# Optimization experiments

Hardware: AMD Instinct MI355X
Metric: run time of the kernel (lower is better)

Reference implementation:

```python
import jax, jax.numpy as jnp
import numpy as np

N, E, D, R = 50000, 625000, 128, 200
BN_EPS = 1e-5


def setup_inputs() -> dict:
    key = jax.random.key(0)
    ks = jax.random.split(key, 16)
    x = jax.random.normal(ks[0], (N, D), dtype=jnp.float32)
    r_feats = jax.random.normal(ks[1], (R, D), dtype=jnp.float32)
    src = jax.random.randint(ks[2], (E,), 0, N, dtype=jnp.int32)
    dst = jax.random.randint(ks[3], (E,), 0, N, dtype=jnp.int32)
    etype = jax.random.randint(ks[4], (E,), 0, R, dtype=jnp.int32)
    norm = jax.random.uniform(ks[5], (E, 1), dtype=jnp.float32)
    out_edges_mask = jax.random.randint(ks[6], (E,), 0, 2) == 1
    in_edges_mask = jnp.logical_not(out_edges_mask)  # masks partition edges
    s = 1.0 / np.sqrt(D)
    def lin(k):
        kw, kb = jax.random.split(k)
        return (jax.random.uniform(kw, (D, D), jnp.float32, -s, s),
                jax.random.uniform(kb, (D,), jnp.float32, -s, s))
    W_O_w, W_O_b = lin(ks[7])
    W_I_w, W_I_b = lin(ks[8])
    W_S_w, W_S_b = lin(ks[9])
    W_R_w, W_R_b = lin(ks[10])
    loop_rel = jax.random.normal(ks[11], (1, D), dtype=jnp.float32) * s  # xavier-ish
    bn_gamma = jnp.ones((D,), jnp.float32)
    bn_beta = jnp.zeros((D,), jnp.float32)
    return {"x": x, "r_feats": r_feats, "src": src, "dst": dst, "etype": etype,
            "norm": norm, "in_edges_mask": in_edges_mask, "out_edges_mask": out_edges_mask,
            "W_O_w": W_O_w, "W_O_b": W_O_b, "W_I_w": W_I_w, "W_I_b": W_I_b,
            "W_S_w": W_S_w, "W_S_b": W_S_b, "W_R_w": W_R_w, "W_R_b": W_R_b,
            "loop_rel": loop_rel, "bn_gamma": bn_gamma, "bn_beta": bn_beta}


def reference(x, r_feats, src, dst, etype, norm, in_edges_mask, out_edges_mask,
              W_O_w, W_O_b, W_I_w, W_I_b, W_S_w, W_S_b, W_R_w, W_R_b,
              loop_rel, bn_gamma, bn_beta):
    # r_feats with self-loop relation appended: [R+1, D]
    r_ext = jnp.concatenate([r_feats, loop_rel], axis=0)
    # per-edge relation feature scaled by norm: [E, D]
    e_h = r_ext[etype] * norm
    # compose (sub): u_sub_e -> src feature minus edge feature
    comp_h = x[src] - e_h
    # per-direction linear projections, selected by the edge partition masks
    h_O = comp_h @ W_O_w.T + W_O_b
    h_I = comp_h @ W_I_w.T + W_I_b
    new_comp_h = jnp.where(out_edges_mask[:, None], h_O, h_I)
    # scatter-sum messages to destination nodes: [N, D]
    agg = jax.ops.segment_sum(new_comp_h, dst, num_segments=x.shape[0])
    # self-loop branch (sub with loop relation)
    comp_h_s = x - r_ext[-1]
    n_out = (comp_h_s @ W_S_w.T + W_S_b + agg) * (1.0 / 3.0)  # dropout in eval mode
    # BatchNorm1d (training-mode batch stats, biased variance)
    mean = jnp.mean(n_out, axis=0)
    var = jnp.mean((n_out - mean) ** 2, axis=0)
    n_out = (n_out - mean) * jax.lax.rsqrt(var + BN_EPS) * bn_gamma + bn_beta
    n_out = jnp.tanh(n_out)
    r_out = r_ext @ W_R_w.T + W_R_b
    return n_out, r_out[:-1]
```

## Files before the change

kernel.cpp:

```cpp
#include <hip/hip_runtime.h>
#include <cstddef>

#define N_NODES 50000
#define N_EDGES 625000
#define DIM     128
#define R_REL   200
#define BN_EPS  1e-5f
#define SLOTS   64

typedef __bf16 bf16x8 __attribute__((ext_vector_type(8)));
typedef float  f32x4  __attribute__((ext_vector_type(4)));

__device__ __forceinline__ float bfu2f(unsigned int hi16) {
    return __uint_as_float(hi16);
}
__device__ __forceinline__ unsigned int f2bfr(float f) {
    unsigned int u = __float_as_uint(f);
    return (u + 0x7fffu + ((u >> 16) & 1u)) >> 16;
}

__global__ void detect_mask_kernel(const unsigned char* __restrict__ in_m,
                                   const unsigned char* __restrict__ out_m,
                                   int* __restrict__ flag) {
    int ok = 1;
    for (int e = 0; e < 256; ++e) ok &= (((int)in_m[e] + (int)out_m[e]) == 1);
    *flag = ok;
}

__global__ __launch_bounds__(256) void tobf16_kernel(const float* __restrict__ in,
                                                     ushort* __restrict__ out, int n4) {
    int i = blockIdx.x * 256 + threadIdx.x;
    if (i < n4) {
        float4 v = ((const float4*)in)[i];
        ushort4 o;
        o.x = (ushort)f2bfr(v.x);
        o.y = (ushort)f2bfr(v.y);
        o.z = (ushort)f2bfr(v.z);
        o.w = (ushort)f2bfr(v.w);
        ((ushort4*)out)[i] = o;
    }
}

__global__ __launch_bounds__(384) void prep_weights_kernel(
    const float* __restrict__ WO, const float* __restrict__ WI,
    const float* __restrict__ WS, ushort* __restrict__ Wb) {
    int f = blockIdx.x;
    int k = threadIdx.x;
    const float third = 1.0f / 3.0f;
    float w;
    if (k < 128)      w = WS[f * DIM + k];
    else if (k < 256) w = WO[f * DIM + (k - 128)];
    else              w = WI[f * DIM + (k - 256)];
    Wb[f * 384 + k] = (ushort)f2bfr(w * third);
}

__global__ void prep_bias_kernel(const float* __restrict__ WS, const float* __restrict__ bS,
                                 const float* __restrict__ bO, const float* __restrict__ bI,
                                 const float* __restrict__ loop,
                                 float* __restrict__ bias0, float* __restrict__ bO3,
                                 float* __restrict__ bI3) {
    int f = threadIdx.x;
    float acc = 0.f;
    for (int k = 0; k < DIM; ++k) acc += loop[k] * WS[f * DIM + k];
    const float third = 1.0f / 3.0f;
    bias0[f] = (bS[f] - acc) * third;
    bO3[f]   = bO[f] * third;
    bI3[f]   = bI[f] * third;
}

__global__ __launch_bounds__(128) void rout_kernel(const float* __restrict__ rf,
                                                   const float* __restrict__ WR,
                                                   const float* __restrict__ bR,
                                                   float* __restrict__ out) {
    int r = blockIdx.x;
    int f = threadIdx.x;
    __shared__ float row[DIM];
    row[f] = rf[r * DIM + f];
    __syncthreads();
    float acc = bR[f];
    for (int k = 0; k < DIM; ++k) acc += row[k] * WR[f * DIM + k];
    out[r * DIM + f] = acc;
}

__global__ __launch_bounds__(256) void slot_fill_kernel(
    const int* __restrict__ dst, const int* __restrict__ src,
    const int* __restrict__ et, const float* __restrict__ norm,
    const void* __restrict__ omask, const int* __restrict__ flag,
    int* __restrict__ cnt, uint2* __restrict__ erec) {
    int e = blockIdx.x * 256 + threadIdx.x;
    if (e >= N_EDGES) return;
    int fl = *flag;
    bool m = fl ? (((const unsigned char*)omask)[e] != 0)
                : (((const int*)omask)[e] != 0);
    int d = dst[e];
    int k = atomicAdd(&cnt[d], 1);
    if (k < SLOTS) {
        unsigned w0 = (unsigned)src[e] | ((unsigned)et[e] << 16) | (m ? 0x80000000u : 0u);
        erec[(size_t)d * SLOTS + k] = make_uint2(w0, (unsigned)__float_as_int(norm[e]));
    }
}

#define AGG_CALC(EX, EY, XW, RW)                                   \
    {                                                              \
        float nm = __uint_as_float(EY);                            \
        float fm = (float)((EX) >> 31);                            \
        float x0 = bfu2f((XW) << 16), x1 = bfu2f((XW) & 0xffff0000u); \
        float r0 = bfu2f((RW) << 16), r1 = bfu2f((RW) & 0xffff0000u); \
        float v0 = __builtin_fmaf(-nm, r0, x0);                    \
        float v1 = __builtin_fmaf(-nm, r1, x1);                    \
        aT0 += v0; aT1 += v1;                                      \
        aO0 = __builtin_fmaf(fm, v0, aO0);                         \
        aO1 = __builtin_fmaf(fm, v1, aO1);                         \
        cOf += fm;                                                 \
    }

__global__ __launch_bounds__(256, 8) void aggregate_kernel(
    const unsigned int* __restrict__ xb,
    const unsigned int* __restrict__ rb,
    const uint2* __restrict__ erec,
    const int* __restrict__ cnt,
    unsigned int* __restrict__ S_Ob, unsigned int* __restrict__ S_Ib,
    float* __restrict__ cntO, float* __restrict__ cntI) {
    int wv = threadIdx.x >> 6;
    unsigned lane = threadIdx.x & 63;
    int n = blockIdx.x * 4 + wv;
    if (n >= N_NODES) return;
    int deg = cnt[n];
    deg = deg < SLOTS ? deg : SLOTS;
    int beg = n * SLOTS, end = beg + deg;

    float aT0 = 0.f, aT1 = 0.f, aO0 = 0.f, aO1 = 0.f, cOf = 0.f;

    int j = beg;
    for (; j + 3 < end; j += 4) {
        uint2 e0 = erec[j], e1 = erec[j + 1], e2 = erec[j + 2], e3 = erec[j + 3];
        unsigned xw0 = xb[((e0.x & 0xffffu) << 6) + lane];
        unsigned rw0 = rb[(((e0.x >> 16) & 0x7fffu) << 6) + lane];
        unsigned xw1 = xb[((e1.x & 0xffffu) << 6) + lane];
        unsigned rw1 = rb[(((e1.x >> 16) & 0x7fffu) << 6) + lane];
        unsigned xw2 = xb[((e2.x & 0xffffu) << 6) + lane];
        unsigned rw2 = rb[(((e2.x >> 16) & 0x7fffu) << 6) + lane];
        unsigned xw3 = xb[((e3.x & 0xffffu) << 6) + lane];
        unsigned rw3 = rb[(((e3.x >> 16) & 0x7fffu) << 6) + lane];
        AGG_CALC(e0.x, e0.y, xw0, rw0)
        AGG_CALC(e1.x, e1.y, xw1, rw1)
        AGG_CALC(e2.x, e2.y, xw2, rw2)
        AGG_CALC(e3.x, e3.y, xw3, rw3)
    }
    for (; j < end; ++j) {
        uint2 e0 = erec[j];
        unsigned xw0 = xb[((e0.x & 0xffffu) << 6) + lane];
        unsigned rw0 = rb[(((e0.x >> 16) & 0x7fffu) << 6) + lane];
        AGG_CALC(e0.x, e0.y, xw0, rw0)
    }

    float aI0 = aT0 - aO0, aI1 = aT1 - aO1;
    S_Ob[((unsigned)n << 6) + lane] = f2bfr(aO0) | (f2bfr(aO1) << 16);
    S_Ib[((unsigned)n << 6) + lane] = f2bfr(aI0) | (f2bfr(aI1) << 16);
    if (lane == 0) { cntO[n] = cOf; cntI[n] = (float)deg - cOf; }
}

__global__ __launch_bounds__(256, 4) void gemm_kernel(
    const ushort* __restrict__ xb, const ushort* __restrict__ S_Ob,
    const ushort* __restrict__ S_Ib, const ushort* __restrict__ Wb,
    const float* __restrict__ bias0, const float* __restrict__ bO3,
    const float* __restrict__ bI3, const float* __restrict__ cntO,
    const float* __restrict__ cntI, float* __restrict__ y,
    float* __restrict__ colsum, float* __restrict__ colsq) {
    __shared__ ushort Bs[128][136];
    __shared__ float redS[4][128];
    __shared__ float redQ[4][128];

    int tid = threadIdx.x;
    int wv = tid >> 6, lane = tid & 63;
    int cl = lane & 15, kg = lane >> 4;
    int wrow0 = blockIdx.x * 64 + wv * 16;

    f32x4 acc[8];
#pragma unroll
    for (int cf = 0; cf < 8; ++cf) acc[cf] = (f32x4){0.f, 0.f, 0.f, 0.f};

    int rowA = wrow0 + cl;
    int rowc = rowA < N_NODES ? rowA : N_NODES - 1;
    const ushort* Abase[3] = {xb, S_Ob, S_Ib};

    for (int kq = 0; kq < 3; ++kq) {
        __syncthreads();
#pragma unroll
        for (int j = 0; j < 8; ++j) {
            int i = tid + j * 256;
            int col = i >> 4, k8 = (i & 15) << 3;
            uint4 w = *(const uint4*)(Wb + (size_t)col * 384 + kq * 128 + k8);
            *(uint4*)&Bs[col][k8] = w;
        }
        const ushort* Ap0 = Abase[kq] + (size_t)rowc * 128 + kg * 8;
        uint4 a4[4];
#pragma unroll
        for (int ks = 0; ks < 4; ++ks) a4[ks] = *(const uint4*)(Ap0 + ks * 32);
        __syncthreads();
#pragma unroll
        for (int ks = 0; ks < 4; ++ks) {
            bf16x8 af = __builtin_bit_cast(bf16x8, a4[ks]);
#pragma unroll
            for (int cf = 0; cf < 8; ++cf) {
                bf16x8 bv = __builtin_bit_cast(bf16x8,
                    *(const uint4*)&Bs[cf * 16 + cl][ks * 32 + kg * 8]);
                acc[cf] = __builtin_amdgcn_mfma_f32_16x16x32_bf16(af, bv, acc[cf], 0, 0, 0);
            }
        }
    }

    float b0a[8], boa[8], bia[8];
#pragma unroll
    for (int cf = 0; cf < 8; ++cf) {
        int col = cf * 16 + cl;
        b0a[cf] = bias0[col]; boa[cf] = bO3[col]; bia[cf] = bI3[col];
    }
    float cOv[4], cIv[4]; int rows[4]; bool rv[4];
#pragma unroll
    for (int r = 0; r < 4; ++r) {
        int row = wrow0 + kg * 4 + r;
        rows[r] = row; rv[r] = row < N_NODES;
        cOv[r] = rv[r] ? cntO[row] : 0.f;
        cIv[r] = rv[r] ? cntI[row] : 0.f;
    }
    float ps[8], pq[8];
#pragma unroll
    for (int cf = 0; cf < 8; ++cf) {
        float s = 0.f, q = 0.f;
        int col = cf * 16 + cl;
#pragma unroll
        for (int r = 0; r < 4; ++r) {
            if (rv[r]) {
                float v = acc[cf][r] + b0a[cf] + cOv[r] * boa[cf] + cIv[r] * bia[cf];
                y[(size_t)rows[r] * DIM + col] = v;
                s += v; q += v * v;
            }
        }
        s += __shfl_xor(s, 16);
        s += __shfl_xor(s, 32);
        q += __shfl_xor(q, 16);
        q += __shfl_xor(q, 32);
        ps[cf] = s; pq[cf] = q;
    }
    if (kg == 0) {
#pragma unroll
        for (int cf = 0; cf < 8; ++cf) {
            redS[wv][cf * 16 + cl] = ps[cf];
            redQ[wv][cf * 16 + cl] = pq[cf];
        }
    }
    __syncthreads();
    if (tid < 128) {
        float s = redS[0][tid] + redS[1][tid] + redS[2][tid] + redS[3][tid];
        float q = redQ[0][tid] + redQ[1][tid] + redQ[2][tid] + redQ[3][tid];
        atomicAdd(colsum + tid, s);
        atomicAdd(colsq + tid, q);
    }
}

__global__ __launch_bounds__(256) void bn_apply_kernel(
    float* __restrict__ y, const float* __restrict__ colsum, const float* __restrict__ colsq,
    const float* __restrict__ gamma, const float* __restrict__ beta) {
    __shared__ __align__(16) float sc[DIM];
    __shared__ __align__(16) float sh[DIM];
    int tid = threadIdx.x;
    if (tid < DIM) {
        float mean = colsum[tid] * (1.0f / N_NODES);
        float var  = colsq[tid] * (1.0f / N_NODES) - mean * mean;
        float s = rsqrtf(var + BN_EPS) * gamma[tid];
        sc[tid] = s;
        sh[tid] = beta[tid] - mean * s;
    }
    __syncthreads();
    const int total4 = N_NODES * 32;
    for (int i = blockIdx.x * 256 + tid; i < total4; i += gridDim.x * 256) {
        float4 s4 = ((const float4*)sc)[i & 31];
        float4 h4 = ((const float4*)sh)[i & 31];
        float4 v = ((float4*)y)[i];
        v.x = tanhf(v.x * s4.x + h4.x);
        v.y = tanhf(v.y * s4.y + h4.y);
        v.z = tanhf(v.z * s4.z + h4.z);
        v.w = tanhf(v.w * s4.w + h4.w);
        ((float4*)y)[i] = v;
    }
}

extern "C" void kernel_launch(void* const* d_in, const int* in_sizes, int n_in,
                              void* d_out, int out_size, void* d_ws, size_t ws_size,
                              hipStream_t stream) {
    const float* x        = (const float*)d_in[0];
    const float* r_feats  = (const float*)d_in[1];
    const int*   src      = (const int*)d_in[2];
    const int*   dst      = (const int*)d_in[3];
    const int*   etype    = (const int*)d_in[4];
    const float* norm     = (const float*)d_in[5];
    const void*  in_mask  = d_in[6];
    const void*  out_mask = d_in[7];
    const float* W_O_w    = (const float*)d_in[8];
    const float* W_O_b    = (const float*)d_in[9];
    const float* W_I_w    = (const float*)d_in[10];
    const float* W_I_b    = (const float*)d_in[11];
    const float* W_S_w    = (const float*)d_in[12];
    const float* W_S_b    = (const float*)d_in[13];
    const float* W_R_w    = (const float*)d_in[14];
    const float* W_R_b    = (const float*)d_in[15];
    const float* loop_rel = (const float*)d_in[16];
    const float* bn_gamma = (const float*)d_in[17];
    const float* bn_beta  = (const float*)d_in[18];

    const size_t ND = (size_t)N_NODES * DIM;
    char* p = (char*)d_ws;
    auto alloc = [&](size_t bytes) { void* r = (void*)p; p += (bytes + 255) & ~(size_t)255; return r; };

    ushort* S_Ob = (ushort*)alloc(ND * 2);
    ushort* S_Ib = (ushort*)alloc(ND * 2);
    ushort* xb   = (ushort*)alloc(ND * 2);
    ushort* rb   = (ushort*)alloc((size_t)R_REL * DIM * 2);
    uint2* erec  = (uint2*)alloc((size_t)N_NODES * SLOTS * 8);
    ushort* Wb   = (ushort*)alloc((size_t)DIM * 384 * 2);
    float* bias0 = (float*)alloc(DIM * 4);
    float* bO3   = (float*)alloc(DIM * 4);
    float* bI3   = (float*)alloc(DIM * 4);
    float* colsum= (float*)alloc(DIM * 4);
    float* colsq = (float*)alloc(DIM * 4);
    float* cntO  = (float*)alloc(N_NODES * 4);
    float* cntI  = (float*)alloc(N_NODES * 4);
    int*   cnt   = (int*)alloc(N_NODES * 4);
    int*   flag  = (int*)alloc(4);

    float* y    = (float*)d_out;
    float* rout = (float*)d_out + ND;

    hipMemsetAsync(cnt, 0, N_NODES * sizeof(int), stream);
    hipMemsetAsync(colsum, 0, DIM * sizeof(float), stream);
    hipMemsetAsync(colsq, 0, DIM * sizeof(float), stream);

    detect_mask_kernel<<<1, 1, 0, stream>>>((const unsigned char*)in_mask,
                                            (const unsigned char*)out_mask, flag);
    tobf16_kernel<<<(int)((ND / 4 + 255) / 256), 256, 0, stream>>>(x, xb, (int)(ND / 4));
    tobf16_kernel<<<(R_REL * DIM / 4 + 255) / 256, 256, 0, stream>>>(r_feats, rb, R_REL * DIM / 4);
    prep_weights_kernel<<<128, 384, 0, stream>>>(W_O_w, W_I_w, W_S_w, Wb);
    prep_bias_kernel<<<1, 128, 0, stream>>>(W_S_w, W_S_b, W_O_b, W_I_b, loop_rel,
                                            bias0, bO3, bI3);
    rout_kernel<<<R_REL, 128, 0, stream>>>(r_feats, W_R_w, W_R_b, rout);

    slot_fill_kernel<<<(N_EDGES + 255) / 256, 256, 0, stream>>>(
        dst, src, etype, norm, out_mask, flag, cnt, erec);

    aggregate_kernel<<<(N_NODES + 3) / 4, 256, 0, stream>>>(
        (const unsigned int*)xb, (const unsigned int*)rb, erec, cnt,
        (unsigned int*)S_Ob, (unsigned int*)S_Ib, cntO, cntI);

    gemm_kernel<<<(N_NODES + 63) / 64, 256, 0, stream>>>(
        xb, S_Ob, S_Ib, Wb, bias0, bO3, bI3, cntO, cntI, y, colsum, colsq);

    bn_apply_kernel<<<2048, 256, 0, stream>>>(y, colsum, colsq, bn_gamma, bn_beta);
}
```

Measured before the change: 155.2 us.

## Fuse setup kernels and memsets; process two nodes per wavefront in aggregation

Replaces three memsets, the mask-detect kernel and two bf16 conversion kernels with one init kernel, and folds the bias prep into the weight-prep kernel with a shared-memory reduction. This cuts the number of launches and serial single-thread work. The aggregation kernel now handles two nodes per 64-lane wavefront, each half-wave loading 8-byte uint2 chunks, so gathers are wider and the wavefront count is halved. The cost is divergence when the two nodes in a wavefront have different degrees.

New measurement: 147.6 us. -4.9%, faster.

```diff
diff --git a/kernel.cpp b/kernel.cpp
--- a/kernel.cpp
+++ b/kernel.cpp
@@ -7,6 +7,8 @@
 #define R_REL   200
 #define BN_EPS  1e-5f
 #define SLOTS   64
+#define ND4     ((N_NODES * DIM) / 4)
+#define R4      ((R_REL * DIM) / 4)
 
 typedef __bf16 bf16x8 __attribute__((ext_vector_type(8)));
 typedef float  f32x4  __attribute__((ext_vector_type(4)));
@@ -19,31 +21,46 @@
     return (u + 0x7fffu + ((u >> 16) & 1u)) >> 16;
 }
 
-__global__ void detect_mask_kernel(const unsigned char* __restrict__ in_m,
-                                   const unsigned char* __restrict__ out_m,
-                                   int* __restrict__ flag) {
-    int ok = 1;
-    for (int e = 0; e < 256; ++e) ok &= (((int)in_m[e] + (int)out_m[e]) == 1);
-    *flag = ok;
-}
-
-__global__ __launch_bounds__(256) void tobf16_kernel(const float* __restrict__ in,
-                                                     ushort* __restrict__ out, int n4) {
-    int i = blockIdx.x * 256 + threadIdx.x;
-    if (i < n4) {
-        float4 v = ((const float4*)in)[i];
+__global__ __launch_bounds__(256) void init_kernel(
+    const float* __restrict__ x, ushort* __restrict__ xb,
+    const float* __restrict__ rf, ushort* __restrict__ rb,
+    int* __restrict__ cnt, float* __restrict__ colsum, float* __restrict__ colsq,
+    const unsigned char* __restrict__ in_m, const unsigned char* __restrict__ out_m,
+    int* __restrict__ flag) {
+    int gid = blockIdx.x * 256 + threadIdx.x;
+    int total = gridDim.x * 256;
+    for (int i = gid; i < ND4; i += total) {
+        float4 v = ((const float4*)x)[i];
         ushort4 o;
-        o.x = (ushort)f2bfr(v.x);
-        o.y = (ushort)f2bfr(v.y);
-        o.z = (ushort)f2bfr(v.z);
-        o.w = (ushort)f2bfr(v.w);
-        ((ushort4*)out)[i] = o;
+        o.x = (ushort)f2bfr(v.x); o.y = (ushort)f2bfr(v.y);
+        o.z = (ushort)f2bfr(v.z); o.w = (ushort)f2bfr(v.w);
+        ((ushort4*)xb)[i] = o;
+    }
+    if (gid < R4) {
+        float4 v = ((const float4*)rf)[gid];
+        ushort4 o;
+        o.x = (ushort)f2bfr(v.x); o.y = (ushort)f2bfr(v.y);
+        o.z = (ushort)f2bfr(v.z); o.w = (ushort)f2bfr(v.w);
+        ((ushort4*)rb)[gid] = o;
+    }
+    for (int i = gid; i < N_NODES; i += total) cnt[i] = 0;
+    if (gid < DIM) { colsum[gid] = 0.f; colsq[gid] = 0.f; }
+    if (blockIdx.x == 0) {
+        int ok = (((int)in_m[threadIdx.x] + (int)out_m[threadIdx.x]) == 1) ? 1 : 0;
+        __shared__ int sred[4];
+        unsigned long long b = __ballot(ok);
+        if ((threadIdx.x & 63) == 0) sred[threadIdx.x >> 6] = (b == ~0ULL) ? 1 : 0;
+        __syncthreads();
+        if (threadIdx.x == 0) *flag = sred[0] & sred[1] & sred[2] & sred[3];
     }
 }
 
 __global__ __launch_bounds__(384) void prep_weights_kernel(
     const float* __restrict__ WO, const float* __restrict__ WI,
-    const float* __restrict__ WS, ushort* __restrict__ Wb) {
+    const float* __restrict__ WS, const float* __restrict__ loop,
+    const float* __restrict__ bS, const float* __restrict__ bO,
+    const float* __restrict__ bI, ushort* __restrict__ Wb,
+    float* __restrict__ bias0, float* __restrict__ bO3, float* __restrict__ bI3) {
     int f = blockIdx.x;
     int k = threadIdx.x;
     const float third = 1.0f / 3.0f;
@@ -52,20 +69,16 @@
     else if (k < 256) w = WO[f * DIM + (k - 128)];
     else              w = WI[f * DIM + (k - 256)];
     Wb[f * 384 + k] = (ushort)f2bfr(w * third);
-}
-
-__global__ void prep_bias_kernel(const float* __restrict__ WS, const float* __restrict__ bS,
-                                 const float* __restrict__ bO, const float* __restrict__ bI,
-                                 const float* __restrict__ loop,
-                                 float* __restrict__ bias0, float* __restrict__ bO3,
-                                 float* __restrict__ bI3) {
-    int f = threadIdx.x;
-    float acc = 0.f;
-    for (int k = 0; k < DIM; ++k) acc += loop[k] * WS[f * DIM + k];
-    const float third = 1.0f / 3.0f;
-    bias0[f] = (bS[f] - acc) * third;
-    bO3[f]   = bO[f] * third;
-    bI3[f]   = bI[f] * third;
+    __shared__ float red[128];
+    if (k < 128) red[k] = loop[k] * WS[f * DIM + k];
+    __syncthreads();
+    for (int off = 64; off; off >>= 1) {
+        if (k < off) red[k] += red[k + off];
+        __syncthreads();
+    }
+    if (k == 0)   bias0[f] = (bS[f] - red[0]) * third;
+    if (k == 64)  bO3[f] = bO[f] * third;
+    if (k == 128) bI3[f] = bI[f] * third;
 }
 
 __global__ __launch_bounds__(128) void rout_kernel(const float* __restrict__ rf,
@@ -100,64 +113,83 @@
     }
 }
 
-#define AGG_CALC(EX, EY, XW, RW)                                   \
-    {                                                              \
-        float nm = __uint_as_float(EY);                            \
-        float fm = (float)((EX) >> 31);                            \
-        float x0 = bfu2f((XW) << 16), x1 = bfu2f((XW) & 0xffff0000u); \
-        float r0 = bfu2f((RW) << 16), r1 = bfu2f((RW) & 0xffff0000u); \
-        float v0 = __builtin_fmaf(-nm, r0, x0);                    \
-        float v1 = __builtin_fmaf(-nm, r1, x1);                    \
-        aT0 += v0; aT1 += v1;                                      \
-        aO0 = __builtin_fmaf(fm, v0, aO0);                         \
-        aO1 = __builtin_fmaf(fm, v1, aO1);                         \
-        cOf += fm;                                                 \
+#define AGG4(E, XW, RW)                                              \
+    {                                                                \
+        float nm = __uint_as_float((E).y);                           \
+        float fm = (float)((E).x >> 31);                             \
+        float x0 = bfu2f((XW).x << 16), x1 = bfu2f((XW).x & 0xffff0000u); \
+        float x2 = bfu2f((XW).y << 16), x3 = bfu2f((XW).y & 0xffff0000u); \
+        float r0 = bfu2f((RW).x << 16), r1 = bfu2f((RW).x & 0xffff0000u); \
+        float r2 = bfu2f((RW).y << 16), r3 = bfu2f((RW).y & 0xffff0000u); \
+        float v0 = __builtin_fmaf(-nm, r0, x0);                      \
+        float v1 = __builtin_fmaf(-nm, r1, x1);                      \
+        float v2 = __builtin_fmaf(-nm, r2, x2);                      \
+        float v3 = __builtin_fmaf(-nm, r3, x3);                      \
+        aT0 += v0; aT1 += v1; aT2 += v2; aT3 += v3;                  \
+        aO0 = __builtin_fmaf(fm, v0, aO0);                           \
+        aO1 = __builtin_fmaf(fm, v1, aO1);                           \
+        aO2 = __builtin_fmaf(fm, v2, aO2);                           \
+        aO3 = __builtin_fmaf(fm, v3, aO3);                           \
+        cOf += fm;                                                   \
     }
 
 __global__ __launch_bounds__(256, 8) void aggregate_kernel(
-    const unsigned int* __restrict__ xb,
-    const unsigned int* __restrict__ rb,
+    const uint2* __restrict__ xb2,
+    const uint2* __restrict__ rb2,
     const uint2* __restrict__ erec,
     const int* __restrict__ cnt,
-    unsigned int* __restrict__ S_Ob, unsigned int* __restrict__ S_Ib,
+    uint2* __restrict__ S_Ob, uint2* __restrict__ S_Ib,
     float* __restrict__ cntO, float* __restrict__ cntI) {
     int wv = threadIdx.x >> 6;
-    unsigned lane = threadIdx.x & 63;
-    int n = blockIdx.x * 4 + wv;
-    if (n >= N_NODES) return;
-    int deg = cnt[n];
-    deg = deg < SLOTS ? deg : SLOTS;
-    int beg = n * SLOTS, end = beg + deg;
-
-    float aT0 = 0.f, aT1 = 0.f, aO0 = 0.f, aO1 = 0.f, cOf = 0.f;
-
-    int j = beg;
-    for (; j + 3 < end; j += 4) {
-        uint2 e0 = erec[j], e1 = erec[j + 1], e2 = erec[j + 2], e3 = erec[j + 3];
-        unsigned xw0 = xb[((e0.x & 0xffffu) << 6) + lane];
-        unsigned rw0 = rb[(((e0.x >> 16) & 0x7fffu) << 6) + lane];
-        unsigned xw1 = xb[((e1.x & 0xffffu) << 6) + lane];
-        unsigned rw1 = rb[(((e1.x >> 16) & 0x7fffu) << 6) + lane];
-        unsigned xw2 = xb[((e2.x & 0xffffu) << 6) + lane];
-        unsigned rw2 = rb[(((e2.x >> 16) & 0x7fffu) << 6) + lane];
-        unsigned xw3 = xb[((e3.x & 0xffffu) << 6) + lane];
-        unsigned rw3 = rb[(((e3.x >> 16) & 0x7fffu) << 6) + lane];
-        AGG_CALC(e0.x, e0.y, xw0, rw0)
-        AGG_CALC(e1.x, e1.y, xw1, rw1)
-        AGG_CALC(e2.x, e2.y, xw2, rw2)
-        AGG_CALC(e3.x, e3.y, xw3, rw3)
-    }
-    for (; j < end; ++j) {
-        uint2 e0 = erec[j];
-        unsigned xw0 = xb[((e0.x & 0xffffu) << 6) + lane];
-        unsigned rw0 = rb[(((e0.x >> 16) & 0x7fffu) << 6) + lane];
-        AGG_CALC(e0.x, e0.y, xw0, rw0)
-    }
-
-    float aI0 = aT0 - aO0, aI1 = aT1 - aO1;
-    S_Ob[((unsigned)n << 6) + lane] = f2bfr(aO0) | (f2bfr(aO1) << 16);
-    S_Ib[((unsigned)n << 6) + lane] = f2bfr(aI0) | (f2bfr(aI1) << 16);
-    if (lane == 0) { cntO[n] = cOf; cntI[n] = (float)deg - cOf; }
+    int lane = threadIdx.x & 63;
+    unsigned l5 = lane & 31;
+    int half = lane >> 5;
+    int n = (blockIdx.x * 4 + wv) * 2 + half;
+    bool valid = n < N_NODES;
+    int deg = 0;
+    if (valid) { deg = cnt[n]; deg = deg < SLOTS ? deg : SLOTS; }
+    int other = __shfl_xor(deg, 32);
+    int mdeg = deg > other ? deg : other;
+    unsigned base = (unsigned)n * SLOTS;
+
+    float aT0 = 0.f, aT1 = 0.f, aT2 = 0.f, aT3 = 0.f;
+    float aO0 = 0.f, aO1 = 0.f, aO2 = 0.f, aO3 = 0.f, cOf = 0.f;
+
+    int j = 0;
+    for (; j + 1 < mdeg; j += 2) {
+        bool a0 = j < deg, a1 = j + 1 < deg;
+        uint2 e0, e1, xw0, rw0, xw1, rw1;
+        if (a0) e0 = erec[base + j];
+        if (a1) e1 = erec[base + j + 1];
+        if (a0) {
+            xw0 = xb2[((e0.x & 0xffffu) << 5) + l5];
+            rw0 = rb2[(((e0.x >> 16) & 0x7fffu) << 5) + l5];
+        }
+        if (a1) {
+            xw1 = xb2[((e1.x & 0xffffu) << 5) + l5];
+            rw1 = rb2[(((e1.x >> 16) & 0x7fffu) << 5) + l5];
+        }
+        if (a0) AGG4(e0, xw0, rw0)
+        if (a1) AGG4(e1, xw1, rw1)
+    }
+    if (j < deg) {
+        uint2 e0 = erec[base + j];
+        uint2 xw0 = xb2[((e0.x & 0xffffu) << 5) + l5];
+        uint2 rw0 = rb2[(((e0.x >> 16) & 0x7fffu) << 5) + l5];
+        AGG4(e0, xw0, rw0)
+    }
+
+    if (valid) {
+        float aI0 = aT0 - aO0, aI1 = aT1 - aO1, aI2 = aT2 - aO2, aI3 = aT3 - aO3;
+        uint2 so, si;
+        so.x = f2bfr(aO0) | (f2bfr(aO1) << 16);
+        so.y = f2bfr(aO2) | (f2bfr(aO3) << 16);
+        si.x = f2bfr(aI0) | (f2bfr(aI1) << 16);
+        si.y = f2bfr(aI2) | (f2bfr(aI3) << 16);
+        S_Ob[((unsigned)n << 5) + l5] = so;
+        S_Ib[((unsigned)n << 5) + l5] = si;
+        if (l5 == 0) { cntO[n] = cOf; cntI[n] = (float)deg - cOf; }
+    }
 }
 
 __global__ __launch_bounds__(256, 4) void gemm_kernel(
@@ -332,25 +364,22 @@
     float* y    = (float*)d_out;
     float* rout = (float*)d_out + ND;
 
-    hipMemsetAsync(cnt, 0, N_NODES * sizeof(int), stream);
-    hipMemsetAsync(colsum, 0, DIM * sizeof(float), stream);
-    hipMemsetAsync(colsq, 0, DIM * sizeof(float), stream);
-
-    detect_mask_kernel<<<1, 1, 0, stream>>>((const unsigned char*)in_mask,
-                                            (const unsigned char*)out_mask, flag);
-    tobf16_kernel<<<(int)((ND / 4 + 255) / 256), 256, 0, stream>>>(x, xb, (int)(ND / 4));
-    tobf16_kernel<<<(R_REL * DIM / 4 + 255) / 256, 256, 0, stream>>>(r_feats, rb, R_REL * DIM / 4);
-    prep_weights_kernel<<<128, 384, 0, stream>>>(W_O_w, W_I_w, W_S_w, Wb);
-    prep_bias_kernel<<<1, 128, 0, stream>>>(W_S_w, W_S_b, W_O_b, W_I_b, loop_rel,
-                                            bias0, bO3, bI3);
+    init_kernel<<<6250, 256, 0, stream>>>(
+        x, xb, r_feats, rb, cnt, colsum, colsq,
+        (const unsigned char*)in_mask, (const unsigned char*)out_mask, flag);
+
+    prep_weights_kernel<<<128, 384, 0, stream>>>(
+        W_O_w, W_I_w, W_S_w, loop_rel, W_S_b, W_O_b, W_I_b,
+        Wb, bias0, bO3, bI3);
+
     rout_kernel<<<R_REL, 128, 0, stream>>>(r_feats, W_R_w, W_R_b, rout);
 
     slot_fill_kernel<<<(N_EDGES + 255) / 256, 256, 0, stream>>>(
         dst, src, etype, norm, out_mask, flag, cnt, erec);
 
-    aggregate_kernel<<<(N_NODES + 3) / 4, 256, 0, stream>>>(
-        (const unsigned int*)xb, (const unsigned int*)rb, erec, cnt,
-        (unsigned int*)S_Ob, (unsigned int*)S_Ib, cntO, cntI);
+    aggregate_kernel<<<(N_NODES + 7) / 8, 256, 0, stream>>>(
+        (const uint2*)xb, (const uint2*)rb, erec, cnt,
+        (uint2*)S_Ob, (uint2*)S_Ib, cntO, cntI);
 
     gemm_kernel<<<(N_NODES + 63) / 64, 256, 0, stream>>>(
         xb, S_Ob, S_Ib, Wb, bias0, bO3, bI3, cntO, cntI, y, colsum, colsq);
```
